# Kernel optimization log

Hardware: AMD Instinct MI355X
Metric: run time of the kernel (lower is better)

The kernel has to match this reference:

```python
import jax, jax.numpy as jnp
import numpy as np

B, N, C, H, F = 8, 1024, 128, 4, 32  # batch, nodes, in_channels, heads, n_hidden
EDGE_P = 0.05


def setup_inputs() -> dict:
    key = jax.random.key(0)
    k1, k2, k3, k4 = jax.random.split(key, 4)
    x = jax.random.normal(k1, (B, N, C), dtype=jnp.float32)
    # torch Linear(in=C, out=H*F, bias=False); stored transposed so x @ W works
    W = jax.random.normal(k2, (C, H * F), dtype=jnp.float32) * (1.0 / np.sqrt(C))
    # attn Linear(2F -> 1, bias=False), single weight vector shared across heads
    a = jax.random.normal(k3, (2 * F,), dtype=jnp.float32) * (1.0 / np.sqrt(2 * F))
    # binary adjacency with self-loops so every row has at least one neighbor
    adj = (jax.random.uniform(k4, (N, N)) < EDGE_P).astype(jnp.int32)
    adj = jnp.maximum(adj, jnp.eye(N, dtype=jnp.int32))
    return {"x": x, "W": W, "a": a, "adj": adj}


def reference(x, W, a, adj):
    b, n, _ = x.shape
    f = a.shape[0] // 2
    h = W.shape[1] // f
    g = (x @ W).reshape(b, n, h, f)                      # (B,N,H,F)
    # attn(cat[g_i, g_j]) decomposes exactly: e_ij = lrelu(a1.g_i + a2.g_j)
    s_i = jnp.einsum('bihf,f->bih', g, a[:f])            # source-node term
    s_j = jnp.einsum('bjhf,f->bjh', g, a[f:])            # neighbor term
    e = jax.nn.leaky_relu(s_i[:, :, None, :] + s_j[:, None, :, :],
                          negative_slope=0.2)            # (B,N,N,H)
    e = jnp.where(adj[None, :, :, None] == 0, -jnp.inf, e)
    att = jax.nn.softmax(e, axis=2)                      # softmax over neighbors j
    out = jnp.einsum('bijh,bjhf->bihf', att, g)          # aggregate neighbors
    return out.reshape(b, n, h * f)                      # is_concat=True
```

## Files before the change

### kernel.cpp

```cpp
#include <hip/hip_runtime.h>
#include <hip/hip_bf16.h>
#include <math.h>

#define GB 8
#define GN 1024
#define GC 128
#define GH 4
#define GF 32
#define GHF 128
#define MAXNBR 192
#define XS_LD 129

__global__ __launch_bounds__(256) void gat_gemm(
    const float* __restrict__ x, const float* __restrict__ W,
    const float* __restrict__ a, const int* __restrict__ adj,
    float* __restrict__ g, float* __restrict__ s1, float* __restrict__ s2,
    int* __restrict__ nbrl, int* __restrict__ cntl) {
  __shared__ float xs[64 * XS_LD];
  __shared__ float red1[4][64];
  __shared__ float red2[4][64];
  const int t = threadIdx.x;
  const int strip = blockIdx.x >> 3;
  const int cb = blockIdx.x & 7;
  const int base = strip * 64;
  const int w = t >> 6, lane = t & 63;

  const float4* __restrict__ x4 = (const float4*)x;
#pragma unroll
  for (int v = t; v < 64 * 32; v += 256) {
    float4 val = x4[base * 32 + v];
    const int r = v >> 5, k4 = (v & 31) * 4;
    xs[r * XS_LD + k4 + 0] = val.x;
    xs[r * XS_LD + k4 + 1] = val.y;
    xs[r * XS_LD + k4 + 2] = val.z;
    xs[r * XS_LD + k4 + 3] = val.w;
  }
  __syncthreads();

  int c0 = cb * 16 + w * 4;
  c0 = __builtin_amdgcn_readfirstlane(c0);
  const int row = base + lane;

  float acc0 = 0.f, acc1 = 0.f, acc2 = 0.f, acc3 = 0.f;
#pragma unroll 8
  for (int k = 0; k < GC; ++k) {
    const float xv = xs[lane * XS_LD + k];
    const float4 wv = *(const float4*)(W + k * GHF + c0);
    acc0 = fmaf(xv, wv.x, acc0);
    acc1 = fmaf(xv, wv.y, acc1);
    acc2 = fmaf(xv, wv.z, acc2);
    acc3 = fmaf(xv, wv.w, acc3);
  }
  *(float4*)(g + (size_t)row * GHF + c0) = make_float4(acc0, acc1, acc2, acc3);

  const int f0 = c0 & (GF - 1);
  const float v1 = acc0 * a[f0] + acc1 * a[f0 + 1] + acc2 * a[f0 + 2] + acc3 * a[f0 + 3];
  const float v2 = acc0 * a[GF + f0] + acc1 * a[GF + f0 + 1] +
                   acc2 * a[GF + f0 + 2] + acc3 * a[GF + f0 + 3];
  red1[w][lane] = v1;
  red2[w][lane] = v2;
  __syncthreads();

  const int h = cb >> 1;
  if (w == 0) {
    float r1 = red1[0][lane] + red1[1][lane] + red1[2][lane] + red1[3][lane];
    atomicAdd(&s1[(size_t)row * GH + h], r1);
  } else if (w == 1) {
    float r2 = red2[0][lane] + red2[1][lane] + red2[2][lane] + red2[3][lane];
    atomicAdd(&s2[(size_t)row * GH + h], r2);
  } else if (w == 3) {
    const int node = blockIdx.x;
    const int* __restrict__ arow = adj + node * GN;
    int* __restrict__ nrow = nbrl + node * MAXNBR;
    int pos0 = 0;
    for (int j0 = 0; j0 < GN; j0 += 64) {
      int v = arow[j0 + lane];
      unsigned long long m = __ballot(v != 0);
      if (v) {
        int pos = pos0 + __popcll(m & ((1ull << lane) - 1ull));
        if (pos < MAXNBR) nrow[pos] = j0 + lane;
      }
      pos0 += __popcll(m);
    }
    if (lane == 0) cntl[node] = min(pos0, MAXNBR);
  }
}

__global__ __launch_bounds__(256) void gat_attn(
    const float* __restrict__ g, const float* __restrict__ s1,
    const float* __restrict__ s2, const int* __restrict__ nbrl,
    const int* __restrict__ cntl, float* __restrict__ out) {
  const int bi = blockIdx.x;
  const int b = bi >> 10;
  const int i = bi & (GN - 1);
  const int t = threadIdx.x;
  const int h = t >> 6, lane = t & 63;

  __shared__ float2 pj[GH][MAXNBR];

  const int count = cntl[i];
  const int jr0 = nbrl[i * MAXNBR + lane];
  const int jr1 = nbrl[i * MAXNBR + lane + 64];
  const int jr2 = nbrl[i * MAXNBR + lane + 128];

  const float si = s1[(size_t)bi * GH + h];
  const float* __restrict__ s2b = s2 + (size_t)b * GN * GH;
  const float* __restrict__ gb = g + (size_t)b * GN * GHF;

  float p0 = 0.f, p1 = 0.f, p2 = 0.f;
  if (lane < count)       { float e = si + s2b[jr0 * GH + h]; e = e > 0.f ? e : 0.2f * e; p0 = __expf(e); }
  if (lane + 64 < count)  { float e = si + s2b[jr1 * GH + h]; e = e > 0.f ? e : 0.2f * e; p1 = __expf(e); }
  if (lane + 128 < count) { float e = si + s2b[jr2 * GH + h]; e = e > 0.f ? e : 0.2f * e; p2 = __expf(e); }
  float s = p0 + p1 + p2;
#pragma unroll
  for (int mk = 32; mk; mk >>= 1) s += __shfl_xor(s, mk);

  pj[h][lane]       = make_float2(p0, __int_as_float(jr0));
  pj[h][lane + 64]  = make_float2(p1, __int_as_float(jr1));
  if (lane < MAXNBR - 128) pj[h][lane + 128] = make_float2(p2, __int_as_float(jr2));

  const int kslot = lane >> 3;
  const int f4 = lane & 7;
  float4 acc = make_float4(0.f, 0.f, 0.f, 0.f);
  for (int k = kslot; k < count; k += 8) {
    const float2 v = pj[h][k];
    const int j = __float_as_int(v.y);
    const float pv = v.x;
    const float4 gv = *(const float4*)&gb[(j * GH + h) * GF + f4 * 4];
    acc.x = fmaf(pv, gv.x, acc.x);
    acc.y = fmaf(pv, gv.y, acc.y);
    acc.z = fmaf(pv, gv.z, acc.z);
    acc.w = fmaf(pv, gv.w, acc.w);
  }
#pragma unroll
  for (int mk = 8; mk <= 32; mk <<= 1) {
    acc.x += __shfl_xor(acc.x, mk);
    acc.y += __shfl_xor(acc.y, mk);
    acc.z += __shfl_xor(acc.z, mk);
    acc.w += __shfl_xor(acc.w, mk);
  }
  if (kslot == 0) {
    const float inv = 1.f / s;
    *(float4*)&out[((size_t)bi * GH + h) * GF + f4 * 4] =
        make_float4(acc.x * inv, acc.y * inv, acc.z * inv, acc.w * inv);
  }
}

extern "C" void kernel_launch(void* const* d_in, const int* in_sizes, int n_in,
                              void* d_out, int out_size, void* d_ws, size_t ws_size,
                              hipStream_t stream) {
  const float* x = (const float*)d_in[0];
  const float* W = (const float*)d_in[1];
  const float* a = (const float*)d_in[2];
  const int* adj = (const int*)d_in[3];
  float* out = (float*)d_out;

  float* ws = (float*)d_ws;
  float* g = ws;
  float* s1 = g + (size_t)GB * GN * GH * GF;
  float* s2 = s1 + (size_t)GB * GN * GH;
  int* nbrl = (int*)(s2 + (size_t)GB * GN * GH);
  int* cntl = nbrl + (size_t)GN * MAXNBR;

  hipMemsetAsync(s1, 0, 2 * (size_t)GB * GN * GH * sizeof(float), stream);

  gat_gemm<<<GN, 256, 0, stream>>>(x, W, a, adj, g, s1, s2, nbrl, cntl);
  gat_attn<<<GB * GN, 256, 0, stream>>>(g, s1, s2, nbrl, cntl, out);
}
```

Measured before the change: 103.8 us.

## Give each GEMM block a full head to drop atomics and memset

```diff
diff --git a/kernel.cpp b/kernel.cpp
--- a/kernel.cpp
+++ b/kernel.cpp
@@ -20,8 +20,8 @@
   __shared__ float red1[4][64];
   __shared__ float red2[4][64];
   const int t = threadIdx.x;
-  const int strip = blockIdx.x >> 3;
-  const int cb = blockIdx.x & 7;
+  const int strip = blockIdx.x >> 2;
+  const int h = blockIdx.x & 3;
   const int base = strip * 64;
   const int w = t >> 6, lane = t & 63;
 
@@ -37,39 +37,50 @@
   }
   __syncthreads();
 
-  int c0 = cb * 16 + w * 4;
+  int c0 = h * 32 + w * 8;
   c0 = __builtin_amdgcn_readfirstlane(c0);
   const int row = base + lane;
 
-  float acc0 = 0.f, acc1 = 0.f, acc2 = 0.f, acc3 = 0.f;
+  float acc[8];
+#pragma unroll
+  for (int q = 0; q < 8; ++q) acc[q] = 0.f;
+
 #pragma unroll 8
   for (int k = 0; k < GC; ++k) {
     const float xv = xs[lane * XS_LD + k];
-    const float4 wv = *(const float4*)(W + k * GHF + c0);
-    acc0 = fmaf(xv, wv.x, acc0);
-    acc1 = fmaf(xv, wv.y, acc1);
-    acc2 = fmaf(xv, wv.z, acc2);
-    acc3 = fmaf(xv, wv.w, acc3);
+    const float4 wa = *(const float4*)(W + k * GHF + c0);
+    const float4 wb = *(const float4*)(W + k * GHF + c0 + 4);
+    acc[0] = fmaf(xv, wa.x, acc[0]);
+    acc[1] = fmaf(xv, wa.y, acc[1]);
+    acc[2] = fmaf(xv, wa.z, acc[2]);
+    acc[3] = fmaf(xv, wa.w, acc[3]);
+    acc[4] = fmaf(xv, wb.x, acc[4]);
+    acc[5] = fmaf(xv, wb.y, acc[5]);
+    acc[6] = fmaf(xv, wb.z, acc[6]);
+    acc[7] = fmaf(xv, wb.w, acc[7]);
   }
-  *(float4*)(g + (size_t)row * GHF + c0) = make_float4(acc0, acc1, acc2, acc3);
+  *(float4*)(g + (size_t)row * GHF + c0) = make_float4(acc[0], acc[1], acc[2], acc[3]);
+  *(float4*)(g + (size_t)row * GHF + c0 + 4) = make_float4(acc[4], acc[5], acc[6], acc[7]);
 
-  const int f0 = c0 & (GF - 1);
-  const float v1 = acc0 * a[f0] + acc1 * a[f0 + 1] + acc2 * a[f0 + 2] + acc3 * a[f0 + 3];
-  const float v2 = acc0 * a[GF + f0] + acc1 * a[GF + f0 + 1] +
-                   acc2 * a[GF + f0 + 2] + acc3 * a[GF + f0 + 3];
+  const int f0 = w * 8;
+  float v1 = 0.f, v2 = 0.f;
+#pragma unroll
+  for (int q = 0; q < 8; ++q) {
+    v1 = fmaf(acc[q], a[f0 + q], v1);
+    v2 = fmaf(acc[q], a[GF + f0 + q], v2);
+  }
   red1[w][lane] = v1;
   red2[w][lane] = v2;
   __syncthreads();
 
-  const int h = cb >> 1;
   if (w == 0) {
-    float r1 = red1[0][lane] + red1[1][lane] + red1[2][lane] + red1[3][lane];
-    atomicAdd(&s1[(size_t)row * GH + h], r1);
+    s1[(size_t)row * GH + h] =
+        red1[0][lane] + red1[1][lane] + red1[2][lane] + red1[3][lane];
   } else if (w == 1) {
-    float r2 = red2[0][lane] + red2[1][lane] + red2[2][lane] + red2[3][lane];
-    atomicAdd(&s2[(size_t)row * GH + h], r2);
-  } else if (w == 3) {
-    const int node = blockIdx.x;
+    s2[(size_t)row * GH + h] =
+        red2[0][lane] + red2[1][lane] + red2[2][lane] + red2[3][lane];
+  } else {
+    const int node = (blockIdx.x << 1) | (w - 2);
     const int* __restrict__ arow = adj + node * GN;
     int* __restrict__ nrow = nbrl + node * MAXNBR;
     int pos0 = 0;
@@ -99,25 +110,46 @@
   __shared__ float2 pj[GH][MAXNBR];
 
   const int count = cntl[i];
-  const int jr0 = nbrl[i * MAXNBR + lane];
-  const int jr1 = nbrl[i * MAXNBR + lane + 64];
-  const int jr2 = nbrl[i * MAXNBR + lane + 128];
-
   const float si = s1[(size_t)bi * GH + h];
   const float* __restrict__ s2b = s2 + (size_t)b * GN * GH;
   const float* __restrict__ gb = g + (size_t)b * GN * GHF;
 
-  float p0 = 0.f, p1 = 0.f, p2 = 0.f;
-  if (lane < count)       { float e = si + s2b[jr0 * GH + h]; e = e > 0.f ? e : 0.2f * e; p0 = __expf(e); }
-  if (lane + 64 < count)  { float e = si + s2b[jr1 * GH + h]; e = e > 0.f ? e : 0.2f * e; p1 = __expf(e); }
-  if (lane + 128 < count) { float e = si + s2b[jr2 * GH + h]; e = e > 0.f ? e : 0.2f * e; p2 = __expf(e); }
-  float s = p0 + p1 + p2;
+  float s;
+  {
+    const int jr0 = nbrl[i * MAXNBR + lane];
+    float p0 = 0.f;
+    if (lane < count) {
+      float e = si + s2b[jr0 * GH + h];
+      e = e > 0.f ? e : 0.2f * e;
+      p0 = __expf(e);
+    }
+    pj[h][lane] = make_float2(p0, __int_as_float(jr0));
+    s = p0;
+  }
+  if (count > 64) {
+    const int jr1 = nbrl[i * MAXNBR + lane + 64];
+    float p1 = 0.f;
+    if (lane + 64 < count) {
+      float e = si + s2b[jr1 * GH + h];
+      e = e > 0.f ? e : 0.2f * e;
+      p1 = __expf(e);
+    }
+    pj[h][lane + 64] = make_float2(p1, __int_as_float(jr1));
+    s += p1;
+  }
+  if (count > 128) {
+    const int jr2 = nbrl[i * MAXNBR + lane + 128];
+    float p2 = 0.f;
+    if (lane + 128 < count) {
+      float e = si + s2b[jr2 * GH + h];
+      e = e > 0.f ? e : 0.2f * e;
+      p2 = __expf(e);
+    }
+    if (lane < MAXNBR - 128) pj[h][lane + 128] = make_float2(p2, __int_as_float(jr2));
+    s += p2;
+  }
 #pragma unroll
   for (int mk = 32; mk; mk >>= 1) s += __shfl_xor(s, mk);
-
-  pj[h][lane]       = make_float2(p0, __int_as_float(jr0));
-  pj[h][lane + 64]  = make_float2(p1, __int_as_float(jr1));
-  if (lane < MAXNBR - 128) pj[h][lane + 128] = make_float2(p2, __int_as_float(jr2));
 
   const int kslot = lane >> 3;
   const int f4 = lane & 7;
@@ -162,8 +194,6 @@
   int* nbrl = (int*)(s2 + (size_t)GB * GN * GH);
   int* cntl = nbrl + (size_t)GN * MAXNBR;
 
-  hipMemsetAsync(s1, 0, 2 * (size_t)GB * GN * GH * sizeof(float), stream);
-
-  gat_gemm<<<GN, 256, 0, stream>>>(x, W, a, adj, g, s1, s2, nbrl, cntl);
+  gat_gemm<<<GN / 2, 256, 0, stream>>>(x, W, a, adj, g, s1, s2, nbrl, cntl);
   gat_attn<<<GB * GN, 256, 0, stream>>>(g, s1, s2, nbrl, cntl, out);
 }
```

Result: faster. 101.1 us (-2.6%).
